# Optimization experiments

Measured on AMD Instinct MI355X. Metric: run time of the kernel, lower is better.

The kernel has to match this reference:

```python
import jax, jax.numpy as jnp
import numpy as np

K = 3  # kernel size along the folded height sub-dimension

def setup_inputs() -> dict:
    key = jax.random.key(0)
    k1, k2 = jax.random.split(key)
    x = jax.random.normal(k1, (1, 48, 56, 56), dtype=jnp.float32)
    W = jax.random.normal(k2, (192, 48, 3), dtype=jnp.float32)
    return {"x": x, "W": W}

def reference(x, W):
    # x: (1,48,56,56) -> (1,48,8,7,56): split H=56 into (8,7)
    t = x.reshape(1, 48, 8, 7, 56)
    # unfold((3,1), padding=(1,0)) acting on the size-7 axis:
    # pad by 1 on each side, then gather K=3 shifted views.
    tp = jnp.pad(t, ((0, 0), (0, 0), (0, 0), (1, 1), (0, 0)))  # (1,48,8,9,56)
    # patches[l,j,n,k,o,m] = tp[l,j,n,o+k,m], o in [0,7), k in [0,3)
    patches = jnp.stack([tp[:, :, :, k:k + 7, :] for k in range(K)], axis=3)  # (1,48,8,3,7,56)
    # einsum 'ljnkom, ijk -> linom' with W (192,48,3)
    out = jnp.einsum('ljnkom,ijk->linom', patches, W)  # (1,192,8,7,56)
    return out.reshape(1, 192, 56, 56)
```

## Files before the change

kernel.cpp:

```cpp
#include <hip/hip_runtime.h>


#define CH_IN 48
#define CH_OUT 192
#define HW 56
#define SP 3136
#define OB 7
#define M4 14
#define SEGS 16
#define JSEG 3
#define BCOL 8
#define IG 4
#define CG 14
#define WST 144

__device__ __forceinline__ void fma4(float4& a, float s, const float4& b) {
    a.x += s * b.x; a.y += s * b.y; a.z += s * b.z; a.w += s * b.w;
}
__device__ __forceinline__ void add4(float4& a, const float4& b) {
    a.x += b.x; a.y += b.y; a.z += b.z; a.w += b.w;
}

__global__ __launch_bounds__(256, 4) void conv_rs_kernel(const float* __restrict__ x,
                                                         const float* __restrict__ W,
                                                         float* __restrict__ out) {
    __shared__ float4 red[SEGS][2][OB][BCOL + 1];
    __shared__ float4 wlds[IG][CH_IN];

    const int tid = threadIdx.x;
    const int c   = tid & (BCOL - 1);
    const int seg = (tid >> 3) & (SEGS - 1);
    const int rg  = tid >> 7;
    const int ig4 = blockIdx.x / CG;
    const int cg  = blockIdx.x % CG;
    const int i0  = ig4 * IG;

    {
        const float* wsrc = W + i0 * WST;
        float* wf = reinterpret_cast<float*>(&wlds[0][0]);
        for (int f = tid; f < IG * WST; f += 256) {
            const int jg = f / 3;
            const int k  = f - jg * 3;
            wf[jg * 4 + k] = wsrc[f];
        }
    }

    const int col = cg * BCOL + c;
    const int n   = col / M4;
    const int m4  = col - n * M4;

    const float* xcol = x + seg * (JSEG * SP) + n * (OB * HW) + m4 * 4;

    float4 acc[IG][4];
#pragma unroll
    for (int ig = 0; ig < IG; ++ig)
#pragma unroll
        for (int o = 0; o < 4; ++o) acc[ig][o] = make_float4(0.f, 0.f, 0.f, 0.f);

    __syncthreads();

    if (rg == 0) {
#pragma unroll 1
        for (int j = 0; j < JSEG; ++j) {
            const float* xj = xcol + j * SP;
            float4 xv[5];
#pragma unroll
            for (int r = 0; r < 5; ++r)
                xv[r] = *reinterpret_cast<const float4*>(xj + r * HW);
#pragma unroll
            for (int ig = 0; ig < IG; ++ig) {
                const float4 w = wlds[ig][seg * JSEG + j];
                const float w0 = w.x, w1 = w.y, w2 = w.z;
#pragma unroll
                for (int o = 0; o < 4; ++o) {
                    if (o > 0) fma4(acc[ig][o], w0, xv[o - 1]);
                    fma4(acc[ig][o], w1, xv[o]);
                    fma4(acc[ig][o], w2, xv[o + 1]);
                }
            }
        }
    } else {
#pragma unroll 1
        for (int j = 0; j < JSEG; ++j) {
            const float* xj = xcol + j * SP;
            float4 xv[4];
#pragma unroll
            for (int r = 0; r < 4; ++r)
                xv[r] = *reinterpret_cast<const float4*>(xj + (3 + r) * HW);
#pragma unroll
            for (int ig = 0; ig < IG; ++ig) {
                const float4 w = wlds[ig][seg * JSEG + j];
                const float w0 = w.x, w1 = w.y, w2 = w.z;
#pragma unroll
                for (int o2 = 0; o2 < 3; ++o2) {
                    fma4(acc[ig][o2], w0, xv[o2]);
                    fma4(acc[ig][o2], w1, xv[o2 + 1]);
                    if (o2 < 2) fma4(acc[ig][o2], w2, xv[o2 + 2]);
                }
            }
        }
    }

#pragma unroll
    for (int p = 0; p < 2; ++p) {
        __syncthreads();
#pragma unroll
        for (int d = 0; d < 2; ++d) {
            const int ch = 2 * p + d;
            if (rg == 0) {
#pragma unroll
                for (int o = 0; o < 4; ++o) red[seg][d][o][c] = acc[ch][o];
            } else {
#pragma unroll
                for (int o2 = 0; o2 < 3; ++o2) red[seg][d][4 + o2][c] = acc[ch][o2];
            }
        }
        __syncthreads();

        if (tid < 2 * OB * BCOL) {
            const int d  = tid / (OB * BCOL);
            const int r  = tid % (OB * BCOL);
            const int o  = r / BCOL;
            const int cc = r % BCOL;
            float4 s = red[0][d][o][cc];
#pragma unroll
            for (int sg = 1; sg < SEGS; ++sg) add4(s, red[sg][d][o][cc]);

            const int col2 = cg * BCOL + cc;
            const int n2   = col2 / M4;
            const int m42  = col2 % M4;
            *reinterpret_cast<float4*>(out + (i0 + 2 * p + d) * SP + n2 * (OB * HW) + o * HW + m42 * 4) = s;
        }
    }
}

extern "C" void kernel_launch(void* const* d_in, const int* in_sizes, int n_in,
                              void* d_out, int out_size, void* d_ws, size_t ws_size,
                              hipStream_t stream) {
    const float* x = (const float*)d_in[0];
    const float* W = (const float*)d_in[1];
    float* out = (float*)d_out;

    const int grid = (CH_OUT / IG) * CG;
    conv_rs_kernel<<<grid, 256, 0, stream>>>(x, W, out);
}
```

Baseline: 61.17 us.

## Split rows across four wavefronts and reduce input segments with warp shuffles

New measurement: 62.90 us. 2.8% more time.

```diff
diff --git a/kernel.cpp b/kernel.cpp
--- a/kernel.cpp
+++ b/kernel.cpp
@@ -7,8 +7,8 @@
 #define SP 3136
 #define OB 7
 #define M4 14
-#define SEGS 16
-#define JSEG 3
+#define SEGS 8
+#define JSEG 6
 #define BCOL 8
 #define IG 4
 #define CG 14
@@ -17,20 +17,22 @@
 __device__ __forceinline__ void fma4(float4& a, float s, const float4& b) {
     a.x += s * b.x; a.y += s * b.y; a.z += s * b.z; a.w += s * b.w;
 }
-__device__ __forceinline__ void add4(float4& a, const float4& b) {
-    a.x += b.x; a.y += b.y; a.z += b.z; a.w += b.w;
+__device__ __forceinline__ void red_xor(float4& a, int mask) {
+    a.x += __shfl_xor(a.x, mask, 64);
+    a.y += __shfl_xor(a.y, mask, 64);
+    a.z += __shfl_xor(a.z, mask, 64);
+    a.w += __shfl_xor(a.w, mask, 64);
 }
 
-__global__ __launch_bounds__(256, 4) void conv_rs_kernel(const float* __restrict__ x,
+__global__ __launch_bounds__(256, 4) void conv_bf_kernel(const float* __restrict__ x,
                                                          const float* __restrict__ W,
                                                          float* __restrict__ out) {
-    __shared__ float4 red[SEGS][2][OB][BCOL + 1];
     __shared__ float4 wlds[IG][CH_IN];
 
     const int tid = threadIdx.x;
     const int c   = tid & (BCOL - 1);
     const int seg = (tid >> 3) & (SEGS - 1);
-    const int rg  = tid >> 7;
+    const int rg  = tid >> 6;
     const int ig4 = blockIdx.x / CG;
     const int cg  = blockIdx.x % CG;
     const int i0  = ig4 * IG;
@@ -50,86 +52,107 @@
     const int m4  = col - n * M4;
 
     const float* xcol = x + seg * (JSEG * SP) + n * (OB * HW) + m4 * 4;
+    const int wj0 = seg * JSEG;
 
-    float4 acc[IG][4];
+    float4 acc[IG][2];
 #pragma unroll
-    for (int ig = 0; ig < IG; ++ig)
-#pragma unroll
-        for (int o = 0; o < 4; ++o) acc[ig][o] = make_float4(0.f, 0.f, 0.f, 0.f);
+    for (int ig = 0; ig < IG; ++ig) {
+        acc[ig][0] = make_float4(0.f, 0.f, 0.f, 0.f);
+        acc[ig][1] = make_float4(0.f, 0.f, 0.f, 0.f);
+    }
 
     __syncthreads();
 
     if (rg == 0) {
-#pragma unroll 1
+#pragma unroll 2
         for (int j = 0; j < JSEG; ++j) {
             const float* xj = xcol + j * SP;
-            float4 xv[5];
-#pragma unroll
-            for (int r = 0; r < 5; ++r)
-                xv[r] = *reinterpret_cast<const float4*>(xj + r * HW);
+            const float4 r0 = *reinterpret_cast<const float4*>(xj + 0 * HW);
+            const float4 r1 = *reinterpret_cast<const float4*>(xj + 1 * HW);
+            const float4 r2 = *reinterpret_cast<const float4*>(xj + 2 * HW);
 #pragma unroll
             for (int ig = 0; ig < IG; ++ig) {
-                const float4 w = wlds[ig][seg * JSEG + j];
-                const float w0 = w.x, w1 = w.y, w2 = w.z;
+                const float4 w = wlds[ig][wj0 + j];
+                fma4(acc[ig][0], w.y, r0);
+                fma4(acc[ig][0], w.z, r1);
+                fma4(acc[ig][1], w.x, r0);
+                fma4(acc[ig][1], w.y, r1);
+                fma4(acc[ig][1], w.z, r2);
+            }
+        }
+    } else if (rg == 1) {
+#pragma unroll 2
+        for (int j = 0; j < JSEG; ++j) {
+            const float* xj = xcol + j * SP;
+            const float4 r1 = *reinterpret_cast<const float4*>(xj + 1 * HW);
+            const float4 r2 = *reinterpret_cast<const float4*>(xj + 2 * HW);
+            const float4 r3 = *reinterpret_cast<const float4*>(xj + 3 * HW);
+            const float4 r4 = *reinterpret_cast<const float4*>(xj + 4 * HW);
 #pragma unroll
-                for (int o = 0; o < 4; ++o) {
-                    if (o > 0) fma4(acc[ig][o], w0, xv[o - 1]);
-                    fma4(acc[ig][o], w1, xv[o]);
-                    fma4(acc[ig][o], w2, xv[o + 1]);
-                }
+            for (int ig = 0; ig < IG; ++ig) {
+                const float4 w = wlds[ig][wj0 + j];
+                fma4(acc[ig][0], w.x, r1);
+                fma4(acc[ig][0], w.y, r2);
+                fma4(acc[ig][0], w.z, r3);
+                fma4(acc[ig][1], w.x, r2);
+                fma4(acc[ig][1], w.y, r3);
+                fma4(acc[ig][1], w.z, r4);
+            }
+        }
+    } else if (rg == 2) {
+#pragma unroll 2
+        for (int j = 0; j < JSEG; ++j) {
+            const float* xj = xcol + j * SP;
+            const float4 r3 = *reinterpret_cast<const float4*>(xj + 3 * HW);
+            const float4 r4 = *reinterpret_cast<const float4*>(xj + 4 * HW);
+            const float4 r5 = *reinterpret_cast<const float4*>(xj + 5 * HW);
+            const float4 r6 = *reinterpret_cast<const float4*>(xj + 6 * HW);
+#pragma unroll
+            for (int ig = 0; ig < IG; ++ig) {
+                const float4 w = wlds[ig][wj0 + j];
+                fma4(acc[ig][0], w.x, r3);
+                fma4(acc[ig][0], w.y, r4);
+                fma4(acc[ig][0], w.z, r5);
+                fma4(acc[ig][1], w.x, r4);
+                fma4(acc[ig][1], w.y, r5);
+                fma4(acc[ig][1], w.z, r6);
             }
         }
     } else {
-#pragma unroll 1
+#pragma unroll 2
         for (int j = 0; j < JSEG; ++j) {
             const float* xj = xcol + j * SP;
-            float4 xv[4];
-#pragma unroll
-            for (int r = 0; r < 4; ++r)
-                xv[r] = *reinterpret_cast<const float4*>(xj + (3 + r) * HW);
+            const float4 r5 = *reinterpret_cast<const float4*>(xj + 5 * HW);
+            const float4 r6 = *reinterpret_cast<const float4*>(xj + 6 * HW);
 #pragma unroll
             for (int ig = 0; ig < IG; ++ig) {
-                const float4 w = wlds[ig][seg * JSEG + j];
-                const float w0 = w.x, w1 = w.y, w2 = w.z;
-#pragma unroll
-                for (int o2 = 0; o2 < 3; ++o2) {
-                    fma4(acc[ig][o2], w0, xv[o2]);
-                    fma4(acc[ig][o2], w1, xv[o2 + 1]);
-                    if (o2 < 2) fma4(acc[ig][o2], w2, xv[o2 + 2]);
-                }
+                const float4 w = wlds[ig][wj0 + j];
+                fma4(acc[ig][0], w.x, r5);
+                fma4(acc[ig][0], w.y, r6);
             }
         }
     }
 
 #pragma unroll
-    for (int p = 0; p < 2; ++p) {
-        __syncthreads();
+    for (int ig = 0; ig < IG; ++ig) {
+        red_xor(acc[ig][0], 8);
+        red_xor(acc[ig][0], 16);
+        red_xor(acc[ig][0], 32);
+        if (rg < 3) {
+            red_xor(acc[ig][1], 8);
+            red_xor(acc[ig][1], 16);
+            red_xor(acc[ig][1], 32);
+        }
+    }
+
+    if (seg == 0) {
+        float* op = out + n * (OB * HW) + (rg * 2) * HW + m4 * 4;
 #pragma unroll
-        for (int d = 0; d < 2; ++d) {
-            const int ch = 2 * p + d;
-            if (rg == 0) {
-#pragma unroll
-                for (int o = 0; o < 4; ++o) red[seg][d][o][c] = acc[ch][o];
-            } else {
-#pragma unroll
-                for (int o2 = 0; o2 < 3; ++o2) red[seg][d][4 + o2][c] = acc[ch][o2];
-            }
-        }
-        __syncthreads();
-
-        if (tid < 2 * OB * BCOL) {
-            const int d  = tid / (OB * BCOL);
-            const int r  = tid % (OB * BCOL);
-            const int o  = r / BCOL;
-            const int cc = r % BCOL;
-            float4 s = red[0][d][o][cc];
-#pragma unroll
-            for (int sg = 1; sg < SEGS; ++sg) add4(s, red[sg][d][o][cc]);
-
-            const int col2 = cg * BCOL + cc;
-            const int n2   = col2 / M4;
-            const int m42  = col2 % M4;
-            *reinterpret_cast<float4*>(out + (i0 + 2 * p + d) * SP + n2 * (OB * HW) + o * HW + m42 * 4) = s;
+        for (int ig = 0; ig < IG; ++ig) {
+            float* oi = op + (i0 + ig) * SP;
+            *reinterpret_cast<float4*>(oi) = acc[ig][0];
+            if (rg < 3)
+                *reinterpret_cast<float4*>(oi + HW) = acc[ig][1];
         }
     }
 }
@@ -142,5 +165,5 @@
     float* out = (float*)d_out;
 
     const int grid = (CH_OUT / IG) * CG;
-    conv_rs_kernel<<<grid, 256, 0, stream>>>(x, W, out);
+    conv_bf_kernel<<<grid, 256, 0, stream>>>(x, W, out);
 }
```
